# Kernel tuning notes

Measured on AMD Instinct MI355X. Metric: run time of the kernel, lower is better.

## Reference

```python
import jax, jax.numpy as jnp
import numpy as np

B, S, D = 8, 4096, 1024
E = 64            # num_experts
K = 2             # top-k
CAP_F = 1.25      # capacity_factor
TEMP = 0.1        # temperature buffer
Z_COEF = 1e-4
LB_COEF = 1e-4


def setup_inputs() -> dict:
    key = jax.random.key(0)
    kx, k1, k2 = jax.random.split(key, 3)
    x = jax.random.normal(kx, (B, S, D), dtype=jnp.float32)
    W1 = jax.random.normal(k1, (D, D // 2), dtype=jnp.float32) * 0.02
    ln_gamma = jnp.ones((D // 2,), dtype=jnp.float32)
    ln_beta = jnp.zeros((D // 2,), dtype=jnp.float32)
    W2 = jax.random.normal(k2, (D // 2, E), dtype=jnp.float32) * 0.02
    return {"x": x, "W1": W1, "ln_gamma": ln_gamma, "ln_beta": ln_beta, "W2": W2}


def _router_logits(x2, W1, ln_gamma, ln_beta, W2):
    h = x2 @ W1                                   # [T, D//2]
    mu = h.mean(-1, keepdims=True)
    var = h.var(-1, keepdims=True)                # biased var, as torch LayerNorm
    h = (h - mu) / jnp.sqrt(var + 1e-5) * ln_gamma + ln_beta
    h = jax.nn.relu(h)
    logits = h @ W2                               # [T, E]
    logits = jnp.clip(logits, -50.0, 50.0)
    nrm = jnp.linalg.norm(logits, axis=-1, keepdims=True)
    return logits / (jnp.maximum(nrm, 1e-6) + 1e-6)


def reference(x, W1, ln_gamma, ln_beta, W2):
    T = x.shape[0] * x.shape[1]
    x2 = x.reshape(T, -1)
    logits = _router_logits(x2, W1, ln_gamma, ln_beta, W2)   # [T, E]
    routing_weights = jax.nn.softmax(logits / TEMP, axis=-1)

    # top-k + weight renormalization (no_grad in original)
    tw, ti = jax.lax.top_k(routing_weights, K)               # [T, K]
    tw = jnp.clip(tw, 1e-3, 0.8)
    tw = tw / (jnp.maximum(tw.sum(-1, keepdims=True), 1e-6) + 1e-6)
    tw = jax.lax.stop_gradient(tw)
    ti = jax.lax.stop_gradient(ti)

    capacity = CAP_F * T * K / E
    counts = jnp.zeros((E,), dtype=jnp.float32)
    dispatch = jnp.zeros((T, E), dtype=jnp.float32)
    rows = jnp.arange(T)
    for kk in range(K):  # fixed small loop over k, matches sequential scatter semantics
        e = ti[:, kk]                                        # [T] expert ids
        m = counts[e] < capacity                             # capacity check vs pre-step counts
        counts = counts + jax.ops.segment_sum(m.astype(jnp.float32), e, num_segments=E)
        cur = dispatch[rows, e]
        dispatch = dispatch.at[rows, e].set(jnp.where(m, tw[:, kk], cur))

    unrouted = dispatch.sum(-1) == 0                         # [T]
    least_loaded = jnp.argmax(capacity - counts)
    dispatch = jnp.where(unrouted[:, None] & (jnp.arange(E) == least_loaded)[None, :], 1.0, dispatch)
    ndm = dispatch / jnp.maximum(dispatch.sum(-1, keepdims=True), 1e-12)
    ndm = jax.lax.stop_gradient(ndm)

    # training losses
    lp = jnp.clip(jax.nn.log_softmax(logits, axis=-1), -50.0, 50.0)
    z_loss = jnp.minimum(jnp.mean(lp * lp), 100.0)
    usage = ndm.sum(0)
    usage = usage / (jnp.maximum(usage.sum(), 1e-6) + 1e-6)
    usage = jnp.clip(usage, 1e-6, 1.0)
    target = jnp.full((E,), 1.0 / E, dtype=jnp.float32)
    # F.kl_div(log(usage+1e-6), target, reduction='batchmean') on 1-D -> divide by E
    kl = jnp.sum(target * (jnp.log(target) - jnp.log(usage + 1e-6))) / E
    kl = jnp.minimum(kl, 100.0)
    loss = Z_COEF * z_loss + LB_COEF * kl
    loss = jnp.where(jnp.isnan(loss) | jnp.isinf(loss), jnp.float32(0.1), loss)

    return jax.lax.stop_gradient(routing_weights), ndm, loss
```

## Files before the change

### kernel.cpp

```cpp
#include <hip/hip_runtime.h>
#include <hip/hip_bf16.h>
#include <math.h>

#define T_TOK 32768
#define D_IN  1024
#define H_DIM 512
#define N_E   64
#define TM    32
#define BK    16
#define CAPACITY 1280
#define MARGIN   2e-4f
#define MARGIN_F 1e-4f
#define KC1 384

#define WS_H    0ull
#define WS_W1P  67108864ull
#define WS_OFF  69206016ull
#define WS_NEED 69900000ull
#define WS_TI0 0
#define WS_TI1 (4*T_TOK)
#define WS_TW0 (8*T_TOK)
#define WS_TW1 (12*T_TOK)
#define WS_CNT (16*T_TOK)
#define WS_USG (WS_CNT+256)
#define WS_FLAGN (WS_USG+256)
#define WS_ZP  (WS_FLAGN+256)
#define WS_FLAGL (WS_ZP+4096)

typedef __attribute__((ext_vector_type(8))) short short8;
typedef __attribute__((ext_vector_type(4))) float f32x4;

__device__ __forceinline__ float wred64(float v){
#pragma unroll
  for (int m=1;m<64;m<<=1) v += __shfl_xor(v, m, 64);
  return v;
}
__device__ __forceinline__ unsigned short f2bf(float f){
  union { __hip_bfloat16 h; unsigned short u; } cv;
  cv.h = __float2bfloat16(f);
  return cv.u;
}
__device__ __forceinline__ float bf2f(unsigned short u){
  union { __hip_bfloat16 h; unsigned short u; } cv;
  cv.u = u;
  return __bfloat162float(cv.h);
}
__device__ __forceinline__ void cvt8(const float4 A, const float4 B, uint4 &hi, uint4 &lo){
  unsigned h0=f2bf(A.x),h1=f2bf(A.y),h2=f2bf(A.z),h3=f2bf(A.w);
  unsigned h4=f2bf(B.x),h5=f2bf(B.y),h6=f2bf(B.z),h7=f2bf(B.w);
  unsigned l0=f2bf(A.x-bf2f(h0)),l1=f2bf(A.y-bf2f(h1)),l2=f2bf(A.z-bf2f(h2)),l3=f2bf(A.w-bf2f(h3));
  unsigned l4=f2bf(B.x-bf2f(h4)),l5=f2bf(B.y-bf2f(h5)),l6=f2bf(B.z-bf2f(h6)),l7=f2bf(B.w-bf2f(h7));
  hi = make_uint4(h0|(h1<<16), h2|(h3<<16), h4|(h5<<16), h6|(h7<<16));
  lo = make_uint4(l0|(l1<<16), l2|(l3<<16), l4|(l5<<16), l6|(l7<<16));
}

__device__ __forceinline__ float np_sum8acc(const float* a, int n){
  float r0=a[0],r1=a[1],r2=a[2],r3=a[3],r4=a[4],r5=a[5],r6=a[6],r7=a[7];
  int lim = n - (n & 7);
  int i = 8;
  for (; i < lim; i += 8){
    r0=__fadd_rn(r0,a[i]);   r1=__fadd_rn(r1,a[i+1]);
    r2=__fadd_rn(r2,a[i+2]); r3=__fadd_rn(r3,a[i+3]);
    r4=__fadd_rn(r4,a[i+4]); r5=__fadd_rn(r5,a[i+5]);
    r6=__fadd_rn(r6,a[i+6]); r7=__fadd_rn(r7,a[i+7]);
  }
  float res=__fadd_rn(__fadd_rn(__fadd_rn(r0,r1),__fadd_rn(r2,r3)),
                      __fadd_rn(__fadd_rn(r4,r5),__fadd_rn(r6,r7)));
  for (; i < n; ++i) res=__fadd_rn(res,a[i]);
  return res;
}
__device__ __forceinline__ float np_sum512(const float* a){
  float s01=__fadd_rn(np_sum8acc(a,128),     np_sum8acc(a+128,128));
  float s23=__fadd_rn(np_sum8acc(a+256,128), np_sum8acc(a+384,128));
  return __fadd_rn(s01,s23);
}

__global__ void k_pack(const float* __restrict__ W1, unsigned short* __restrict__ W1p)
{
  int T = blockIdx.x*256 + threadIdx.x;
  int lane = T & 63;  int rest = T >> 6;
  int nt = rest & 7;  rest >>= 3;
  int s  = rest & 1;  rest >>= 1;
  int ks = rest & 31; int nb = rest >> 5;
  int n  = nb*128 + nt*16 + (lane & 15);
  int kb = ks*32 + (lane >> 4)*8;
  unsigned short o[8];
#pragma unroll
  for (int j=0;j<8;++j){
    float w = W1[(size_t)(kb+j)*H_DIM + n];
    unsigned short hi = f2bf(w);
    o[j] = s ? f2bf(w - bf2f(hi)) : hi;
  }
  size_t base = ((size_t)((((nb*32+ks)*2+s)*8+nt))*512 + (size_t)lane*8);
#pragma unroll
  for (int j=0;j<8;++j) W1p[base+j] = o[j];
}

__launch_bounds__(256, 2)
__global__ void k_g1(const float* __restrict__ x, const unsigned short* __restrict__ W1p,
                     float* __restrict__ h)
{
  __shared__ __align__(16) unsigned short aF[8192];
  __shared__ __align__(16) unsigned short bF[8192];

  const int b   = blockIdx.x;
  const int nbn = (b >> 3) & 3;
  const int bm  = (b & 7) + (b >> 5) * 8;
  const int t0  = bm * 128;

  const int tid  = threadIdx.x;
  const int lane = tid & 63;
  const int wid  = tid >> 6;
  const int wr4  = (wid >> 1) * 4;
  const int wc4  = (wid & 1) * 4;

  const int s0 = tid, s1 = tid + 256;
  const int row0 = ((s0>>6)<<4) + (s0&15);  const int g0 = (s0>>4)&3;
  const int row1 = ((s1>>6)<<4) + (s1&15);  const int g1 = (s1>>4)&3;
  const size_t xoff0 = (size_t)(t0+row0)*D_IN + g0*8;
  const size_t xoff1 = (size_t)(t0+row1)*D_IN + g1*8;

  f32x4 acc[4][4];
#pragma unroll
  for (int m=0;m<4;++m)
#pragma unroll
    for (int n=0;n<4;++n) acc[m][n] = (f32x4){0.f,0.f,0.f,0.f};

  float4 x0a, x0b, x1a, x1b;
  uint4  bb0, bb1, bb2, bb3;

#define LOADG(KS) do {                                                        \
    int k0_ = (KS)*32;                                                        \
    x0a = *(const float4*)&x[xoff0 + k0_];                                    \
    x0b = *(const float4*)&x[xoff0 + k0_ + 4];                                \
    x1a = *(const float4*)&x[xoff1 + k0_];                                    \
    x1b = *(const float4*)&x[xoff1 + k0_ + 4];                                \
    size_t ch_ = (size_t)(nbn*32 + (KS)) * 8192;                              \
    bb0 = *(const uint4*)&W1p[ch_ + (size_t)(0*256+tid)*8];                   \
    bb1 = *(const uint4*)&W1p[ch_ + (size_t)(1*256+tid)*8];                   \
    bb2 = *(const uint4*)&W1p[ch_ + (size_t)(2*256+tid)*8];                   \
    bb3 = *(const uint4*)&W1p[ch_ + (size_t)(3*256+tid)*8];                   \
  } while(0)

#define WRITE() do {                                                          \
    uint4 hi_, lo_;                                                           \
    cvt8(x0a, x0b, hi_, lo_);                                                 \
    *(uint4*)&aF[s0*8]        = hi_;                                          \
    *(uint4*)&aF[4096 + s0*8] = lo_;                                          \
    cvt8(x1a, x1b, hi_, lo_);                                                 \
    *(uint4*)&aF[s1*8]        = hi_;                                          \
    *(uint4*)&aF[4096 + s1*8] = lo_;                                          \
    *(uint4*)&bF[(0*256+tid)*8] = bb0;                                        \
    *(uint4*)&bF[(1*256+tid)*8] = bb1;                                        \
    *(uint4*)&bF[(2*256+tid)*8] = bb2;                                        \
    *(uint4*)&bF[(3*256+tid)*8] = bb3;                                        \
  } while(0)

  LOADG(0);
  WRITE();
  LOADG(1);
  __syncthreads();

  for (int ks=0; ks<32; ++ks){
    short8 ah[4], al[4], bh4[4], bl4[4];
#pragma unroll
    for (int m=0;m<4;++m){
      ah[m] = *(const short8*)&aF[((wr4+m)*64+lane)*8];
      al[m] = *(const short8*)&aF[4096 + ((wr4+m)*64+lane)*8];
    }
#pragma unroll
    for (int n=0;n<4;++n){
      bh4[n] = *(const short8*)&bF[((wc4+n)*64+lane)*8];
      bl4[n] = *(const short8*)&bF[4096 + ((wc4+n)*64+lane)*8];
    }
#pragma unroll
    for (int m=0;m<4;++m)
#pragma unroll
      for (int n=0;n<4;++n){
        acc[m][n] = __builtin_amdgcn_mfma_f32_16x16x32_bf16(ah[m], bh4[n], acc[m][n], 0,0,0);
        acc[m][n] = __builtin_amdgcn_mfma_f32_16x16x32_bf16(al[m], bh4[n], acc[m][n], 0,0,0);
        acc[m][n] = __builtin_amdgcn_mfma_f32_16x16x32_bf16(ah[m], bl4[n], acc[m][n], 0,0,0);
      }
    __syncthreads();
    if (ks < 31) WRITE();
    if (ks < 30) LOADG(ks+2);
    __syncthreads();
  }
#undef LOADG
#undef WRITE

  const int cr = (lane >> 4) * 4;
  const int cc = lane & 15;
#pragma unroll
  for (int m=0;m<4;++m)
#pragma unroll
    for (int n=0;n<4;++n){
      int row0_ = t0 + (wr4+m)*16 + cr;
      int col   = nbn*128 + (wc4+n)*16 + cc;
#pragma unroll
      for (int r=0;r<4;++r)
        h[(size_t)(row0_+r)*H_DIM + col] = acc[m][n][r];
    }
}

__launch_bounds__(256, 3)
__global__ void k_ln2(const float* __restrict__ h,
                      const float* __restrict__ gamma,
                      const float* __restrict__ beta,
                      const float* __restrict__ W2,
                      float* __restrict__ out_rw,
                      int*   __restrict__ ti0, int* __restrict__ ti1,
                      float* __restrict__ tw0, float* __restrict__ tw1,
                      float* __restrict__ zpart,
                      int* __restrict__ flagn, int* __restrict__ flagl,
                      int* __restrict__ counts)
{
  __shared__ __align__(16) char smem[75136];
  __shared__ float zw[4];
  __shared__ int lhist[N_E];
  float* hnT  = (float*)smem;
  float* redS = (float*)(smem + 33792);
  float* redQ = (float*)(smem + 38016);
  float* sW2  = (float*)(smem + 33792);
  float* logitsL = (float*)(smem + 66560);
  float* muA  = (float*)(smem + 74880);
  float* rsA  = (float*)(smem + 75008);

  const int tid  = threadIdx.x;
  const int wv   = tid >> 6;
  const int lane = tid & 63;
  const int tl   = lane & 7;
  const int cl   = lane >> 3;
  const int cbase = wv*128 + cl*16;
  const int t0 = blockIdx.x * TM;

  if (tid < N_E) lhist[tid] = 0;

  float acc[4][16];
#pragma unroll
  for (int j=0;j<4;++j)
#pragma unroll
    for (int q=0;q<4;++q)
      *(float4*)&acc[j][q*4] = *(const float4*)&h[(size_t)(t0+tl*4+j)*H_DIM + cbase + q*4];

  const int g = wv*8 + cl;
#pragma unroll
  for (int j=0;j<4;++j) {
    float s=0.f, qq=0.f;
#pragma unroll
    for (int q=0;q<16;++q){ s += acc[j][q]; qq += acc[j][q]*acc[j][q]; }
    redS[(tl*4+j)*33 + g] = s;
    redQ[(tl*4+j)*33 + g] = qq;
  }
  __syncthreads();
  if (tid < 32) {
    float s=0.f, qq=0.f;
    for (int gg=0; gg<32; ++gg){ s += redS[tid*33+gg]; qq += redQ[tid*33+gg]; }
    float mu = s * (1.f/512.f);
    float var = qq * (1.f/512.f) - mu*mu;
    muA[tid] = mu;
    rsA[tid] = rsqrtf(var + 1e-5f);
  }
  __syncthreads();

  {
    float gmv[16], btv[16];
#pragma unroll
    for (int q=0;q<4;++q){
      *(float4*)&gmv[q*4] = *(const float4*)&gamma[cbase+q*4];
      *(float4*)&btv[q*4] = *(const float4*)&beta[cbase+q*4];
    }
    float mu_[4], rs_[4];
#pragma unroll
    for (int j=0;j<4;++j){ mu_[j]=muA[tl*4+j]; rs_[j]=rsA[tl*4+j]; }
#pragma unroll
    for (int j=0;j<4;++j)
#pragma unroll
      for (int q=0;q<16;++q){
        float hv = (acc[j][q]-mu_[j])*rs_[j]*gmv[q] + btv[q];
        acc[j][q] = fmaxf(hv, 0.f);
      }
  }

  float plog[8];
#pragma unroll
  for (int i=0;i<8;++i) plog[i]=0.f;
  const int t2 = tid & 31, e0 = (tid >> 5) * 8;

  for (int p=0; p<2; ++p) {
    if ((wv>>1) == p) {
      int ccb = (wv&1)*128 + cl*16;
#pragma unroll
      for (int j=0;j<4;++j)
#pragma unroll
        for (int q=0;q<16;++q)
          hnT[(ccb+q)*33 + tl*4 + j] = acc[j][q];
    }
    __syncthreads();
    for (int ch=0; ch<2; ++ch) {
      {
        const float4* src = (const float4*)(W2 + (size_t)(p*256+ch*128)*N_E);
        float4* dst = (float4*)sW2;
#pragma unroll
        for (int i=0;i<8;++i) dst[tid + 256*i] = src[tid + 256*i];
      }
      __syncthreads();
#pragma unroll 8
      for (int kk=0; kk<128; ++kk) {
        float hh = hnT[(ch*128+kk)*33 + t2];
        float4 wa = *(const float4*)&sW2[kk*64 + e0];
        float4 wb = *(const float4*)&sW2[kk*64 + e0 + 4];
        plog[0]=fmaf(hh,wa.x,plog[0]); plog[1]=fmaf(hh,wa.y,plog[1]);
        plog[2]=fmaf(hh,wa.z,plog[2]); plog[3]=fmaf(hh,wa.w,plog[3]);
        plog[4]=fmaf(hh,wb.x,plog[4]); plog[5]=fmaf(hh,wb.y,plog[5]);
        plog[6]=fmaf(hh,wb.z,plog[6]); plog[7]=fmaf(hh,wb.w,plog[7]);
      }
      __syncthreads();
    }
  }
#pragma unroll
  for (int i=0;i<8;++i) logitsL[t2*65 + e0 + i] = plog[i];
  __syncthreads();

  const int tE = tid >> 3, jE = tid & 7;
  float v[8];
#pragma unroll
  for (int i=0;i<8;++i){
    float z = logitsL[tE*65 + jE*8 + i];
    v[i] = fminf(fmaxf(z, -50.f), 50.f);
  }
  float ss = 0.f;
#pragma unroll
  for (int i=0;i<8;++i) ss += v[i]*v[i];
#pragma unroll
  for (int m=1;m<8;m<<=1) ss += __shfl_xor(ss, m, 8);
  float scale = 1.f/(fmaxf(sqrtf(ss), 1e-6f) + 1e-6f);
  float ln[8];
#pragma unroll
  for (int i=0;i<8;++i) ln[i] = v[i]*scale;
  float mx = -1e30f;
#pragma unroll
  for (int i=0;i<8;++i) mx = fmaxf(mx, ln[i]);
#pragma unroll
  for (int m=1;m<8;m<<=1) mx = fmaxf(mx, __shfl_xor(mx, m, 8));

  float ex[8], st=0.f, sn=0.f;
#pragma unroll
  for (int i=0;i<8;++i){
    ex[i] = expf((ln[i]-mx)*10.f);
    st += ex[i];
    sn += expf(ln[i]-mx);
  }
#pragma unroll
  for (int m=1;m<8;m<<=1){ st += __shfl_xor(st, m, 8); sn += __shfl_xor(sn, m, 8); }

  float inv_st = 1.f/st;
  float rw[8];
#pragma unroll
  for (int i=0;i<8;++i) rw[i] = ex[i]*inv_st;

  const size_t tok = (size_t)t0 + tE;
  {
    float4* o = (float4*)(out_rw + tok*N_E + jE*8);
    o[0] = make_float4(rw[0],rw[1],rw[2],rw[3]);
    o[1] = make_float4(rw[4],rw[5],rw[6],rw[7]);
  }

  float g1,g2,g3; int i1,i2;
  {
    float bv=-1e30f; int bi=1<<30;
#pragma unroll
    for (int i=0;i<8;++i){ int idx=jE*8+i;
      if (ln[i]>bv || (ln[i]==bv && idx<bi)){ bv=ln[i]; bi=idx; } }
#pragma unroll
    for (int m=1;m<8;m<<=1){ float ov=__shfl_xor(bv,m,8); int oi=__shfl_xor(bi,m,8);
      if (ov>bv || (ov==bv && oi<bi)){ bv=ov; bi=oi; } }
    g1=bv; i1=bi;
    bv=-1e30f; bi=1<<30;
#pragma unroll
    for (int i=0;i<8;++i){ int idx=jE*8+i; if (idx==i1) continue;
      if (ln[i]>bv || (ln[i]==bv && idx<bi)){ bv=ln[i]; bi=idx; } }
#pragma unroll
    for (int m=1;m<8;m<<=1){ float ov=__shfl_xor(bv,m,8); int oi=__shfl_xor(bi,m,8);
      if (ov>bv || (ov==bv && oi<bi)){ bv=ov; bi=oi; } }
    g2=bv; i2=bi;
    bv=-1e30f;
#pragma unroll
    for (int i=0;i<8;++i){ int idx=jE*8+i; if (idx==i1||idx==i2) continue;
      bv = fmaxf(bv, ln[i]); }
#pragma unroll
    for (int m=1;m<8;m<<=1) bv = fmaxf(bv, __shfl_xor(bv,m,8));
    g3=bv;
  }
  if (jE==0){
    float r1 = expf((g1-mx)*10.f)*inv_st;
    float r2 = expf((g2-mx)*10.f)*inv_st;
    float a1 = fminf(fmaxf(r1, 0.001f), 0.8f);
    float a2 = fminf(fmaxf(r2, 0.001f), 0.8f);
    float d  = fmaxf(a1+a2, 1e-6f) + 1e-6f;
    ti0[tok]=i1; ti1[tok]=i2; tw0[tok]=a1/d; tw1[tok]=a2/d;
    bool flg = ((g1-g2) < MARGIN_F) || ((g2-g3) < MARGIN_F);
    if (flg){
      int p = atomicAdd(flagn, 1);
      flagl[p] = (int)tok;
    } else {
      atomicAdd(&lhist[i1], 1);
    }
  }

  float lse = mx + logf(sn);
  float zq = 0.f;
#pragma unroll
  for (int i=0;i<8;++i){
    float lp = fminf(fmaxf(ln[i]-lse, -50.f), 50.f);
    zq += lp*lp;
  }
  zq = wred64(zq);
  if (lane==0) zw[wv] = zq;
  __syncthreads();
  if (tid==0) zpart[blockIdx.x] = zw[0]+zw[1]+zw[2]+zw[3];
  if (tid < N_E && lhist[tid] > 0) atomicAdd(&counts[tid], lhist[tid]);
}

__launch_bounds__(256, 3)
__global__ void k_main(const float* __restrict__ x,
                       const float* __restrict__ W1,
                       const float* __restrict__ gamma,
                       const float* __restrict__ beta,
                       const float* __restrict__ W2,
                       float* __restrict__ out_rw,
                       int*   __restrict__ ti0, int* __restrict__ ti1,
                       float* __restrict__ tw0, float* __restrict__ tw1,
                       float* __restrict__ zpart,
                       int* __restrict__ flagn, int* __restrict__ flagl)
{
  __shared__ __align__(16) char smem[53888];
  __shared__ float zw[4];
  float* sW   = (float*)smem;
  float* sX   = (float*)(smem + 32768);
  float* hnT  = (float*)smem;
  float* redS = (float*)(smem + 36864);
  float* redQ = (float*)(smem + 36864 + 4224);
  float* sW2  = (float*)(smem + 36864);
  float* logitsL = (float*)(smem + 45312);
  float* muA  = (float*)(smem + 53632);
  float* rsA  = (float*)(smem + 53760);

  const int tid  = threadIdx.x;
  const int wv   = tid >> 6;
  const int lane = tid & 63;
  const int tl   = lane & 7;
  const int cl   = lane >> 3;
  const int cbase = wv*128 + cl*16;
  const int t0 = blockIdx.x * TM;

  float acc[4][16];
#pragma unroll
  for (int j=0;j<4;++j)
#pragma unroll
    for (int q=0;q<16;++q) acc[j][q]=0.f;

  for (int k0 = 0; k0 < D_IN; k0 += BK) {
    {
      const float4* srcw = (const float4*)(W1 + (size_t)k0 * H_DIM);
      float4* dstw = (float4*)sW;
#pragma unroll
      for (int i=0;i<8;++i) dstw[tid + 256*i] = srcw[tid + 256*i];
    }
    {
      int e0 = tid*2;
      int tt = e0 >> 4, kk = e0 & 15;
      float2 xv = *(const float2*)&x[(size_t)(t0+tt)*D_IN + k0 + kk];
      sX[kk*36 + tt]     = xv.x;
      sX[(kk+1)*36 + tt] = xv.y;
    }
    __syncthreads();
#pragma unroll
    for (int kk=0; kk<BK; ++kk) {
      float4 a = *(const float4*)&sX[kk*36 + tl*4];
      float b[16];
#pragma unroll
      for (int q=0;q<4;++q) *(float4*)&b[q*4] = *(const float4*)&sW[kk*512 + cbase + q*4];
      float av[4] = {a.x, a.y, a.z, a.w};
#pragma unroll
      for (int j=0;j<4;++j)
#pragma unroll
        for (int q=0;q<16;++q)
          acc[j][q] = fmaf(av[j], b[q], acc[j][q]);
    }
    __syncthreads();
  }

  const int g = wv*8 + cl;
#pragma unroll
  for (int j=0;j<4;++j) {
    float s=0.f, qq=0.f;
#pragma unroll
    for (int q=0;q<16;++q){ s += acc[j][q]; qq += acc[j][q]*acc[j][q]; }
    redS[(tl*4+j)*33 + g] = s;
    redQ[(tl*4+j)*33 + g] = qq;
  }
  __syncthreads();
  if (tid < 32) {
    float s=0.f, qq=0.f;
    for (int gg=0; gg<32; ++gg){ s += redS[tid*33+gg]; qq += redQ[tid*33+gg]; }
    float mu = s * (1.f/512.f);
    float var = qq * (1.f/512.f) - mu*mu;
    muA[tid] = mu;
    rsA[tid] = rsqrtf(var + 1e-5f);
  }
  __syncthreads();

  {
    float gmv[16], btv[16];
#pragma unroll
    for (int q=0;q<4;++q){
      *(float4*)&gmv[q*4] = *(const float4*)&gamma[cbase+q*4];
      *(float4*)&btv[q*4] = *(const float4*)&beta[cbase+q*4];
    }
    float mu_[4], rs_[4];
#pragma unroll
    for (int j=0;j<4;++j){ mu_[j]=muA[tl*4+j]; rs_[j]=rsA[tl*4+j]; }
#pragma unroll
    for (int j=0;j<4;++j)
#pragma unroll
      for (int q=0;q<16;++q){
        float hv = (acc[j][q]-mu_[j])*rs_[j]*gmv[q] + btv[q];
        acc[j][q] = fmaxf(hv, 0.f);
      }
  }

  float plog[8];
#pragma unroll
  for (int i=0;i<8;++i) plog[i]=0.f;
  const int t2 = tid & 31, e0 = (tid >> 5) * 8;

  for (int p=0; p<2; ++p) {
    if ((wv>>1) == p) {
      int ccb = (wv&1)*128 + cl*16;
#pragma unroll
      for (int j=0;j<4;++j)
#pragma unroll
        for (int q=0;q<16;++q)
          hnT[(ccb+q)*33 + tl*4 + j] = acc[j][q];
    }
    __syncthreads();
    for (int ch=0; ch<8; ++ch) {
      {
        const float4* src = (const float4*)(W2 + (size_t)(p*256+ch*32)*N_E);
        float4* dst = (float4*)sW2;
        dst[tid]     = src[tid];
        dst[tid+256] = src[tid+256];
      }
      __syncthreads();
#pragma unroll
      for (int kk=0; kk<32; ++kk) {
        float hh = hnT[(ch*32+kk)*33 + t2];
        float4 wa = *(const float4*)&sW2[kk*64 + e0];
        float4 wb = *(const float4*)&sW2[kk*64 + e0 + 4];
        plog[0]=fmaf(hh,wa.x,plog[0]); plog[1]=fmaf(hh,wa.y,plog[1]);
        plog[2]=fmaf(hh,wa.z,plog[2]); plog[3]=fmaf(hh,wa.w,plog[3]);
        plog[4]=fmaf(hh,wb.x,plog[4]); plog[5]=fmaf(hh,wb.y,plog[5]);
        plog[6]=fmaf(hh,wb.z,plog[6]); plog[7]=fmaf(hh,wb.w,plog[7]);
      }
      __syncthreads();
    }
  }
#pragma unroll
  for (int i=0;i<8;++i) logitsL[t2*65 + e0 + i] = plog[i];
  __syncthreads();

  const int tE = tid >> 3, jE = tid & 7;
  float v[8];
#pragma unroll
  for (int i=0;i<8;++i){
    float z = logitsL[tE*65 + jE*8 + i];
    v[i] = fminf(fmaxf(z, -50.f), 50.f);
  }
  float ss = 0.f;
#pragma unroll
  for (int i=0;i<8;++i) ss += v[i]*v[i];
#pragma unroll
  for (int m=1;m<8;m<<=1) ss += __shfl_xor(ss, m, 8);
  float scale = 1.f/(fmaxf(sqrtf(ss), 1e-6f) + 1e-6f);
  float ln[8];
#pragma unroll
  for (int i=0;i<8;++i) ln[i] = v[i]*scale;
  float mx = -1e30f;
#pragma unroll
  for (int i=0;i<8;++i) mx = fmaxf(mx, ln[i]);
#pragma unroll
  for (int m=1;m<8;m<<=1) mx = fmaxf(mx, __shfl_xor(mx, m, 8));

  float ex[8], st=0.f, sn=0.f;
#pragma unroll
  for (int i=0;i<8;++i){
    ex[i] = expf((ln[i]-mx)*10.f);
    st += ex[i];
    sn += expf(ln[i]-mx);
  }
#pragma unroll
  for (int m=1;m<8;m<<=1){ st += __shfl_xor(st, m, 8); sn += __shfl_xor(sn, m, 8); }

  float inv_st = 1.f/st;
  float rw[8];
#pragma unroll
  for (int i=0;i<8;++i) rw[i] = ex[i]*inv_st;

  const size_t tok = (size_t)t0 + tE;
  {
    float4* o = (float4*)(out_rw + tok*N_E + jE*8);
    o[0] = make_float4(rw[0],rw[1],rw[2],rw[3]);
    o[1] = make_float4(rw[4],rw[5],rw[6],rw[7]);
  }

  float g1,g2,g3; int i1,i2;
  {
    float bv=-1e30f; int bi=1<<30;
#pragma unroll
    for (int i=0;i<8;++i){ int idx=jE*8+i;
      if (ln[i]>bv || (ln[i]==bv && idx<bi)){ bv=ln[i]; bi=idx; } }
#pragma unroll
    for (int m=1;m<8;m<<=1){ float ov=__shfl_xor(bv,m,8); int oi=__shfl_xor(bi,m,8);
      if (ov>bv || (ov==bv && oi<bi)){ bv=ov; bi=oi; } }
    g1=bv; i1=bi;
    bv=-1e30f; bi=1<<30;
#pragma unroll
    for (int i=0;i<8;++i){ int idx=jE*8+i; if (idx==i1) continue;
      if (ln[i]>bv || (ln[i]==bv && idx<bi)){ bv=ln[i]; bi=idx; } }
#pragma unroll
    for (int m=1;m<8;m<<=1){ float ov=__shfl_xor(bv,m,8); int oi=__shfl_xor(bi,m,8);
      if (ov>bv || (ov==bv && oi<bi)){ bv=ov; bi=oi; } }
    g2=bv; i2=bi;
    bv=-1e30f;
#pragma unroll
    for (int i=0;i<8;++i){ int idx=jE*8+i; if (idx==i1||idx==i2) continue;
      bv = fmaxf(bv, ln[i]); }
#pragma unroll
    for (int m=1;m<8;m<<=1) bv = fmaxf(bv, __shfl_xor(bv,m,8));
    g3=bv;
  }
  if (jE==0){
    float r1 = expf((g1-mx)*10.f)*inv_st;
    float r2 = expf((g2-mx)*10.f)*inv_st;
    float a1 = fminf(fmaxf(r1, 0.001f), 0.8f);
    float a2 = fminf(fmaxf(r2, 0.001f), 0.8f);
    float d  = fmaxf(a1+a2, 1e-6f) + 1e-6f;
    ti0[tok]=i1; ti1[tok]=i2; tw0[tok]=a1/d; tw1[tok]=a2/d;
    if ((g1-g2) < MARGIN || (g2-g3) < MARGIN){
      int p = atomicAdd(flagn, 1);
      flagl[p] = (int)tok;
    }
  }

  float lse = mx + logf(sn);
  float zq = 0.f;
#pragma unroll
  for (int i=0;i<8;++i){
    float lp = fminf(fmaxf(ln[i]-lse, -50.f), 50.f);
    zq += lp*lp;
  }
  zq = wred64(zq);
  if (lane==0) zw[wv] = zq;
  __syncthreads();
  if (tid==0) zpart[blockIdx.x] = zw[0]+zw[1]+zw[2]+zw[3];
}

__launch_bounds__(256, 1)
__global__ void k_fix(const float* __restrict__ x, const float* __restrict__ W1,
                      const float* __restrict__ gamma, const float* __restrict__ beta,
                      const float* __restrict__ W2,
                      const int* __restrict__ flagl, const int* __restrict__ flagn,
                      int* __restrict__ ti0, int* __restrict__ ti1,
                      float* __restrict__ tw0, float* __restrict__ tw1,
                      int* __restrict__ counts, int do_count)
{
  __shared__ __align__(16) float sx[D_IN];
  __shared__ __align__(16) float sW[32*H_DIM];
  __shared__ float hS[H_DIM], sqS[H_DIM], hnS[H_DIM];
  __shared__ float sq64[N_E], eS[N_E];
  __shared__ float sc[4];
  const int tid = threadIdx.x;
  const int nf = *flagn;
  for (int it = blockIdx.x; it < nf; it += gridDim.x) {
    const int tok = flagl[it];
    ((float4*)sx)[tid] = ((const float4*)(x + (size_t)tok*D_IN))[tid];
    const int c0 = tid*2;
    float h0=0.f, h1=0.f, a0=0.f, a1=0.f;
    for (int kb=0; kb<D_IN; kb+=32){
      __syncthreads();
      const float4* src = (const float4*)(W1 + (size_t)kb*H_DIM);
#pragma unroll
      for (int i=0;i<16;++i) ((float4*)sW)[tid + 256*i] = src[tid + 256*i];
      __syncthreads();
#pragma unroll 8
      for (int k=0;k<32;++k){
        float xk = sx[kb+k];
        float2 w = *(const float2*)&sW[k*H_DIM + c0];
        a0 = fmaf(xk, w.x, a0); a1 = fmaf(xk, w.y, a1);
      }
      int ke = kb + 32;
      if (ke == 384){ h0 = a0; h1 = a1; a0 = 0.f; a1 = 0.f; }
      else if (ke == 768 || ke == 1024){
        h0 = __fadd_rn(h0, a0); h1 = __fadd_rn(h1, a1); a0 = 0.f; a1 = 0.f;
      }
    }
    hS[c0]=h0; hS[c0+1]=h1;
    __syncthreads();
    if (tid==0) sc[0] = __fdiv_rn(np_sum512(hS), 512.0f);
    __syncthreads();
    float mu = sc[0];
    float d0 = __fsub_rn(h0, mu), d1 = __fsub_rn(h1, mu);
    sqS[c0]   = __fmul_rn(d0,d0);
    sqS[c0+1] = __fmul_rn(d1,d1);
    __syncthreads();
    if (tid==0){
      float var = __fdiv_rn(np_sum512(sqS), 512.0f);
      sc[1] = __fsqrt_rn(__fadd_rn(var, 1e-5f));
    }
    __syncthreads();
    float den = sc[1];
    float2 gm = *(const float2*)&gamma[c0];
    float2 bt = *(const float2*)&beta[c0];
    hnS[c0]   = fmaxf(__fadd_rn(__fmul_rn(__fdiv_rn(d0,den), gm.x), bt.x), 0.f);
    hnS[c0+1] = fmaxf(__fadd_rn(__fmul_rn(__fdiv_rn(d1,den), gm.y), bt.y), 0.f);
    float b0=0.f, b1=0.f;
    for (int half=0; half<2; ++half){
      __syncthreads();
      const float4* src = (const float4*)(W2 + (size_t)(half*256)*N_E);
#pragma unroll
      for (int i=0;i<16;++i) ((float4*)sW)[tid + 256*i] = src[tid + 256*i];
      __syncthreads();
      if (tid < N_E){
        if (half==0){
#pragma unroll 8
          for (int c=0;c<256;++c) b0 = fmaf(hnS[c], sW[c*N_E+tid], b0);
        } else {
#pragma unroll 8
          for (int c=256;c<KC1;++c) b0 = fmaf(hnS[c], sW[(c-256)*N_E+tid], b0);
#pragma unroll 8
          for (int c=KC1;c<H_DIM;++c) b1 = fmaf(hnS[c], sW[(c-256)*N_E+tid], b1);
        }
      }
    }
    float lgf = 0.f;
    if (tid < N_E){
      lgf = __fadd_rn(b0, b1);
      lgf = fminf(fmaxf(lgf, -50.f), 50.f);
      sq64[tid] = __fmul_rn(lgf, lgf);
    }
    __syncthreads();
    if (tid==0){
      float nrm = __fsqrt_rn(np_sum8acc(sq64, 64));
      sc[2] = __fadd_rn(fmaxf(nrm, 1e-6f), 1e-6f);
    }
    __syncthreads();
    if (tid < N_E){
      float nl = __fdiv_rn(lgf, sc[2]);
      float z  = __fdiv_rn(nl, 0.1f);
      float mz = z;
#pragma unroll
      for (int m=1;m<64;m<<=1) mz = fmaxf(mz, __shfl_xor(mz,m,64));
      eS[tid] = expf(__fsub_rn(z, mz));
    }
    __syncthreads();
    if (tid==0) sc[3] = np_sum8acc(eS, 64);
    __syncthreads();
    if (tid < N_E){
      float rw = __fdiv_rn(eS[tid], sc[3]);
      float bv = rw; int bi = tid;
#pragma unroll
      for (int m=1;m<64;m<<=1){ float ov=__shfl_xor(bv,m,64); int oi=__shfl_xor(bi,m,64);
        if (ov>bv || (ov==bv && oi<bi)){ bv=ov; bi=oi; } }
      float R1=bv; int I1=bi;
      bv = (tid==I1) ? -1.f : rw; bi = (tid==I1) ? (1<<30) : tid;
#pragma unroll
      for (int m=1;m<64;m<<=1){ float ov=__shfl_xor(bv,m,64); int oi=__shfl_xor(bi,m,64);
        if (ov>bv || (ov==bv && oi<bi)){ bv=ov; bi=oi; } }
      float R2=bv; int I2=bi;
      if (tid==0){
        float A1 = fminf(fmaxf(R1, 0.001f), 0.8f);
        float A2 = fminf(fmaxf(R2, 0.001f), 0.8f);
        float dd = __fadd_rn(fmaxf(__fadd_rn(A1,A2), 1e-6f), 1e-6f);
        ti0[tok]=I1; ti1[tok]=I2;
        tw0[tok]=__fdiv_rn(A1,dd); tw1[tok]=__fdiv_rn(A2,dd);
        if (do_count) atomicAdd(&counts[I1], 1);
      }
    }
    __syncthreads();
  }
}

__global__ void k_hist(const int* __restrict__ ti0, int* __restrict__ counts)
{
  __shared__ int lh[N_E];
  int tid = threadIdx.x;
  if (tid < N_E) lh[tid] = 0;
  __syncthreads();
  int i = blockIdx.x*256 + tid;
  atomicAdd(&lh[ti0[i]], 1);
  __syncthreads();
  if (tid < N_E) atomicAdd(&counts[tid], lh[tid]);
}

__global__ void k_dispatch(const int* __restrict__ ti0, const int* __restrict__ ti1,
                           const float* __restrict__ tw0, const float* __restrict__ tw1,
                           const int* __restrict__ counts,
                           float* __restrict__ out_ndm, float* __restrict__ usage)
{
  __shared__ float lus[N_E];
  int tid = threadIdx.x;
  if (tid < N_E) lus[tid] = 0.f;
  __syncthreads();
  int gid = blockIdx.x*256 + tid;
  size_t tok = gid >> 3;
  int jE = gid & 7;
  int i0 = ti0[tok], i1 = ti1[tok];
  float w0 = tw0[tok], w1 = tw1[tok];
  float w1m = (counts[i1] < CAPACITY) ? w1 : 0.f;
  float inv = 1.f / fmaxf(w0 + w1m, 1e-12f);
  float vv[8];
#pragma unroll
  for (int i=0;i<8;++i){
    int e = jE*8+i;
    vv[i] = (e==i0) ? w0*inv : (e==i1) ? w1m*inv : 0.f;
  }
  float4* o = (float4*)(out_ndm + tok*N_E + jE*8);
  o[0] = make_float4(vv[0],vv[1],vv[2],vv[3]);
  o[1] = make_float4(vv[4],vv[5],vv[6],vv[7]);
  if (jE==0){
    atomicAdd(&lus[i0], w0*inv);
    atomicAdd(&lus[i1], w1m*inv);
  }
  __syncthreads();
  if (tid < N_E) atomicAdd(&usage[tid], lus[tid]);
}

__global__ void k_final(const float* __restrict__ usage, const float* __restrict__ zpart,
                        float* __restrict__ out_loss)
{
  int e = threadIdx.x;
  float u = usage[e];
  float usum = wred64(u);
  float un = u / (fmaxf(usum, 1e-6f) + 1e-6f);
  un = fminf(fmaxf(un, 1e-6f), 1.0f);
  const float target = 1.0f/64.0f;
  float term = target * (logf(target) - logf(un + 1e-6f));
  float kl = wred64(term) * (1.0f/64.0f);
  kl = fminf(kl, 100.f);
  float zs = 0.f;
  for (int i=e; i<1024; i+=64) zs += zpart[i];
  zs = wred64(zs);
  float z = fminf(zs / (float)(T_TOK*N_E), 100.f);
  float loss = 1e-4f*z + 1e-4f*kl;
  if (isnan(loss) || isinf(loss)) loss = 0.1f;
  if (e==0) out_loss[0] = loss;
}

extern "C" void kernel_launch(void* const* d_in, const int* in_sizes, int n_in,
                              void* d_out, int out_size, void* d_ws, size_t ws_size,
                              hipStream_t stream) {
  const float* x     = (const float*)d_in[0];
  const float* W1    = (const float*)d_in[1];
  const float* gamma = (const float*)d_in[2];
  const float* beta  = (const float*)d_in[3];
  const float* W2    = (const float*)d_in[4];
  float* out = (float*)d_out;

  const bool fast = (ws_size >= WS_NEED);
  char* ws = (char*)d_ws;
  char* sb = ws + (fast ? WS_OFF : 0ull);
  int*   ti0   = (int*)(sb + WS_TI0);
  int*   ti1   = (int*)(sb + WS_TI1);
  float* tw0   = (float*)(sb + WS_TW0);
  float* tw1   = (float*)(sb + WS_TW1);
  int*   cnts  = (int*)(sb + WS_CNT);
  float* usage = (float*)(sb + WS_USG);
  int*   flagn = (int*)(sb + WS_FLAGN);
  float* zpart = (float*)(sb + WS_ZP);
  int*   flagl = (int*)(sb + WS_FLAGL);

  hipMemsetAsync(sb + WS_CNT, 0, 768, stream);

  float* out_rw   = out;
  float* out_ndm  = out + (size_t)T_TOK*N_E;
  float* out_loss = out + 2ull*T_TOK*N_E;

  if (fast) {
    float* hbuf = (float*)(ws + WS_H);
    unsigned short* W1p = (unsigned short*)(ws + WS_W1P);
    k_pack<<<512, 256, 0, stream>>>(W1, W1p);
    k_g1<<<1024, 256, 0, stream>>>(x, W1p, hbuf);
    k_ln2<<<T_TOK/TM, 256, 0, stream>>>(hbuf, gamma, beta, W2,
                                        out_rw, ti0, ti1, tw0, tw1, zpart,
                                        flagn, flagl, cnts);
    k_fix<<<1024, 256, 0, stream>>>(x, W1, gamma, beta, W2, flagl, flagn,
                                    ti0, ti1, tw0, tw1, cnts, 1);
  } else {
    k_main<<<T_TOK/TM, 256, 0, stream>>>(x, W1, gamma, beta, W2,
                                         out_rw, ti0, ti1, tw0, tw1, zpart,
                                         flagn, flagl);
    k_fix<<<1024, 256, 0, stream>>>(x, W1, gamma, beta, W2, flagl, flagn,
                                    ti0, ti1, tw0, tw1, cnts, 0);
    k_hist<<<T_TOK/256, 256, 0, stream>>>(ti0, cnts);
  }
  k_dispatch<<<(T_TOK*8)/256, 256, 0, stream>>>(ti0, ti1, tw0, tw1, cnts,
                                                out_ndm, usage);
  k_final<<<1, 64, 0, stream>>>(usage, zpart, out_loss);
}
```

Measured before the change: 282.4 us.

## Load x fragments directly into registers in GEMM1, bypassing LDS staging

In the first router GEMM, each wave now loads its own x rows from global memory straight into MFMA fragment layout and converts them to bf16 hi/lo in registers, so the A-operand LDS buffer is gone. Only the W1 tile still goes through shared memory. This removes the LDS writes and reads for A and halves shared-memory use, but each wave column pair now loads the same x rows twice, which doubles global/L2 traffic for x. The prefetch depth also shrinks from two stages to one.

```diff
diff --git a/kernel.cpp b/kernel.cpp
--- a/kernel.cpp
+++ b/kernel.cpp
@@ -53,6 +53,9 @@
   hi = make_uint4(h0|(h1<<16), h2|(h3<<16), h4|(h5<<16), h6|(h7<<16));
   lo = make_uint4(l0|(l1<<16), l2|(l3<<16), l4|(l5<<16), l6|(l7<<16));
 }
+__device__ __forceinline__ short8 u4s8(uint4 v){
+  union { uint4 u; short8 s; } cv; cv.u = v; return cv.s;
+}
 
 __device__ __forceinline__ float np_sum8acc(const float* a, int n){
   float r0=a[0],r1=a[1],r2=a[2],r3=a[3],r4=a[4],r5=a[5],r6=a[6],r7=a[7];
@@ -100,7 +103,6 @@
 __global__ void k_g1(const float* __restrict__ x, const unsigned short* __restrict__ W1p,
                      float* __restrict__ h)
 {
-  __shared__ __align__(16) unsigned short aF[8192];
   __shared__ __align__(16) unsigned short bF[8192];
 
   const int b   = blockIdx.x;
@@ -114,11 +116,12 @@
   const int wr4  = (wid >> 1) * 4;
   const int wc4  = (wid & 1) * 4;
 
-  const int s0 = tid, s1 = tid + 256;
-  const int row0 = ((s0>>6)<<4) + (s0&15);  const int g0 = (s0>>4)&3;
-  const int row1 = ((s1>>6)<<4) + (s1&15);  const int g1 = (s1>>4)&3;
-  const size_t xoff0 = (size_t)(t0+row0)*D_IN + g0*8;
-  const size_t xoff1 = (size_t)(t0+row1)*D_IN + g1*8;
+  const int arow = lane & 15;
+  const int akof = (lane >> 4) * 8;
+  size_t aoff0 = (size_t)(t0 + (wr4+0)*16 + arow)*D_IN + akof;
+  size_t aoff1 = (size_t)(t0 + (wr4+1)*16 + arow)*D_IN + akof;
+  size_t aoff2 = (size_t)(t0 + (wr4+2)*16 + arow)*D_IN + akof;
+  size_t aoff3 = (size_t)(t0 + (wr4+3)*16 + arow)*D_IN + akof;
 
   f32x4 acc[4][4];
 #pragma unroll
@@ -126,15 +129,18 @@
 #pragma unroll
     for (int n=0;n<4;++n) acc[m][n] = (f32x4){0.f,0.f,0.f,0.f};
 
-  float4 x0a, x0b, x1a, x1b;
+  float4 xa0,xb0, xa1,xb1, xa2,xb2, xa3,xb3;
   uint4  bb0, bb1, bb2, bb3;
 
-#define LOADG(KS) do {                                                        \
+#define LOADX(KS) do {                                                        \
     int k0_ = (KS)*32;                                                        \
-    x0a = *(const float4*)&x[xoff0 + k0_];                                    \
-    x0b = *(const float4*)&x[xoff0 + k0_ + 4];                                \
-    x1a = *(const float4*)&x[xoff1 + k0_];                                    \
-    x1b = *(const float4*)&x[xoff1 + k0_ + 4];                                \
+    xa0 = *(const float4*)&x[aoff0 + k0_]; xb0 = *(const float4*)&x[aoff0 + k0_ + 4]; \
+    xa1 = *(const float4*)&x[aoff1 + k0_]; xb1 = *(const float4*)&x[aoff1 + k0_ + 4]; \
+    xa2 = *(const float4*)&x[aoff2 + k0_]; xb2 = *(const float4*)&x[aoff2 + k0_ + 4]; \
+    xa3 = *(const float4*)&x[aoff3 + k0_]; xb3 = *(const float4*)&x[aoff3 + k0_ + 4]; \
+  } while(0)
+
+#define LOADB(KS) do {                                                        \
     size_t ch_ = (size_t)(nbn*32 + (KS)) * 8192;                              \
     bb0 = *(const uint4*)&W1p[ch_ + (size_t)(0*256+tid)*8];                   \
     bb1 = *(const uint4*)&W1p[ch_ + (size_t)(1*256+tid)*8];                   \
@@ -142,32 +148,32 @@
     bb3 = *(const uint4*)&W1p[ch_ + (size_t)(3*256+tid)*8];                   \
   } while(0)
 
-#define WRITE() do {                                                          \
-    uint4 hi_, lo_;                                                           \
-    cvt8(x0a, x0b, hi_, lo_);                                                 \
-    *(uint4*)&aF[s0*8]        = hi_;                                          \
-    *(uint4*)&aF[4096 + s0*8] = lo_;                                          \
-    cvt8(x1a, x1b, hi_, lo_);                                                 \
-    *(uint4*)&aF[s1*8]        = hi_;                                          \
-    *(uint4*)&aF[4096 + s1*8] = lo_;                                          \
+#define WRITEB() do {                                                         \
     *(uint4*)&bF[(0*256+tid)*8] = bb0;                                        \
     *(uint4*)&bF[(1*256+tid)*8] = bb1;                                        \
     *(uint4*)&bF[(2*256+tid)*8] = bb2;                                        \
     *(uint4*)&bF[(3*256+tid)*8] = bb3;                                        \
   } while(0)
 
-  LOADG(0);
-  WRITE();
-  LOADG(1);
+  LOADB(0);
+  WRITEB();
+  LOADX(0);
   __syncthreads();
 
   for (int ks=0; ks<32; ++ks){
-    short8 ah[4], al[4], bh4[4], bl4[4];
-#pragma unroll
-    for (int m=0;m<4;++m){
-      ah[m] = *(const short8*)&aF[((wr4+m)*64+lane)*8];
-      al[m] = *(const short8*)&aF[4096 + ((wr4+m)*64+lane)*8];
-    }
+    short8 ah[4], al[4];
+    {
+      uint4 hi_, lo_;
+      cvt8(xa0, xb0, hi_, lo_); ah[0]=u4s8(hi_); al[0]=u4s8(lo_);
+      cvt8(xa1, xb1, hi_, lo_); ah[1]=u4s8(hi_); al[1]=u4s8(lo_);
+      cvt8(xa2, xb2, hi_, lo_); ah[2]=u4s8(hi_); al[2]=u4s8(lo_);
+      cvt8(xa3, xb3, hi_, lo_); ah[3]=u4s8(hi_); al[3]=u4s8(lo_);
+    }
+    if (ks+1 < 32){
+      LOADX(ks+1);
+      LOADB(ks+1);
+    }
+    short8 bh4[4], bl4[4];
 #pragma unroll
     for (int n=0;n<4;++n){
       bh4[n] = *(const short8*)&bF[((wc4+n)*64+lane)*8];
@@ -182,12 +188,12 @@
         acc[m][n] = __builtin_amdgcn_mfma_f32_16x16x32_bf16(ah[m], bl4[n], acc[m][n], 0,0,0);
       }
     __syncthreads();
-    if (ks < 31) WRITE();
-    if (ks < 30) LOADG(ks+2);
-    __syncthreads();
-  }
-#undef LOADG
-#undef WRITE
+    if (ks+1 < 32) WRITEB();
+    __syncthreads();
+  }
+#undef LOADX
+#undef LOADB
+#undef WRITEB
 
   const int cr = (lane >> 4) * 4;
   const int cc = lane & 15;
```

After: 325.2 us. 1.15x slower.
